# Optimization experiments

Hardware: AMD Instinct MI355X
Metric: run time of the kernel (lower is better)

The kernel has to match this reference:

```python
import jax, jax.numpy as jnp
import numpy as np

H, HKV, D = 16, 4, 64
ROPE_BASE = 10000.0
EPS = 1e-6


def _rms_norm(x):
    return x * jax.lax.rsqrt(jnp.mean(x * x, axis=-1, keepdims=True) + EPS)


def _rope_cos_sin(T, dtype):
    inv_freq = 1.0 / (ROPE_BASE ** (jnp.arange(0, D, 2, dtype=jnp.float32) / D))  # [D/2]
    t = jnp.arange(T, dtype=jnp.float32)
    freqs = jnp.outer(t, inv_freq)  # [T, D/2]
    return jnp.cos(freqs)[None, :, None, :].astype(dtype), jnp.sin(freqs)[None, :, None, :].astype(dtype)


def _apply_rope(x, cos, sin):
    d = x.shape[-1] // 2
    x1, x2 = x[..., :d], x[..., d:]
    return jnp.concatenate([x1 * cos + x2 * sin, -x1 * sin + x2 * cos], axis=-1)


def setup_inputs() -> dict:
    key = jax.random.key(0)
    ks = jax.random.split(key, 6)
    B, T, dm = 1, 2048, 1024
    x = jax.random.normal(ks[0], (B, T, dm), dtype=jnp.float32)
    q_w = jax.random.normal(ks[1], (H * D, dm), dtype=jnp.float32) * 0.02
    k_w = jax.random.normal(ks[2], (HKV * D, dm), dtype=jnp.float32) * 0.02
    v_w = jax.random.normal(ks[3], (HKV * D, dm), dtype=jnp.float32) * 0.02
    o_w = jax.random.normal(ks[4], (dm, H * D), dtype=jnp.float32) * 0.02
    temp = jnp.ones((H,), dtype=jnp.float32) * np.sqrt(D)  # per-head temperature buffer
    curvature = jnp.asarray(1.0, dtype=jnp.float32)
    return {"x": x, "q_w": q_w, "k_w": k_w, "v_w": v_w, "o_w": o_w, "temp": temp, "curvature": curvature}


def reference(x, q_w, k_w, v_w, o_w, temp, curvature):
    B, T, dm = x.shape
    # projections
    q = (x @ q_w.T).reshape(B, T, H, D)
    k = (x @ k_w.T).reshape(B, T, HKV, D)
    v = (x @ v_w.T).reshape(B, T, HKV, D)
    q, k = _rms_norm(q), _rms_norm(k)
    cos, sin = _rope_cos_sin(T, q.dtype)
    q = _apply_rope(q, cos, sin)
    k = _apply_rope(k, cos, sin)
    # GQA: repeat kv heads
    rep = H // HKV
    k = jnp.repeat(k, rep, axis=2)  # [B,T,H,D]
    v = jnp.repeat(v, rep, axis=2)
    c = curvature
    # hyperboloid lift: time component x0 = sqrt(1/c + ||x||^2)
    q0 = jnp.sqrt(1.0 / c + jnp.sum(q * q, axis=-1))  # [B,T,H]
    k0 = jnp.sqrt(1.0 / c + jnp.sum(k * k, axis=-1))
    # Minkowski inner product <q,k>_L = q.k_spatial - q0*k0  -> [B,H,Tq,Tk]
    mink = jnp.einsum('bqhd,bkhd->bhqk', q, k) - q0.transpose(0, 2, 1)[..., :, None] * k0.transpose(0, 2, 1)[..., None, :]
    # Lorentz distance d = arccosh(clamp(-c*<q,k>_L, 1+eps)) / sqrt(c)
    dist = jnp.arccosh(jnp.maximum(-c * mink, 1.0 + 1e-5)) / jnp.sqrt(c)
    scores = -dist / temp[None, :, None, None]
    causal = jnp.tril(jnp.ones((T, T), dtype=bool))
    scores = jnp.where(causal[None, None], scores, -jnp.inf)
    w = jax.nn.softmax(scores, axis=-1)  # [B,H,Tq,Tk]
    attn = jnp.einsum('bhqk,bkhd->bqhd', w, v).reshape(B, T, H * D)
    out = attn @ o_w.T  # [B,T,dm]
    spatial_norm = jnp.mean(jnp.sqrt(jnp.sum(q * q, axis=-1)))
    return out, spatial_norm
```

## Files before the change

kernel.cpp:

```cpp
#include <hip/hip_runtime.h>
#include <hip/hip_bf16.h>

typedef __attribute__((ext_vector_type(8))) short short8;
typedef __attribute__((ext_vector_type(4))) short bf16x4;
typedef __attribute__((ext_vector_type(4))) float f32x4;

#define TT 2048
#define DM 1024
#define NH 16
#define NKV 4
#define HD 64

#define MFMA32(a,b,c) __builtin_amdgcn_mfma_f32_16x16x32_bf16(a,b,c,0,0,0)
#define MFMA16(a,b,c) __builtin_amdgcn_mfma_f32_16x16x16bf16_1k(a,b,c,0,0,0)

__device__ __forceinline__ unsigned short f2bf(float x){
  unsigned int u = __float_as_uint(x);
  u += 0x7fffu + ((u >> 16) & 1u);
  return (unsigned short)(u >> 16);
}
__device__ __forceinline__ unsigned int pkbf2(float x, float y){
  union { __hip_bfloat162 h; unsigned int u; } t;
  t.h = __float22bfloat162_rn(make_float2(x, y));
  return t.u;
}

__global__ __launch_bounds__(256) void convertw_kernel(
    const float* __restrict__ x,
    const float* __restrict__ qw, const float* __restrict__ kw,
    const float* __restrict__ vw, const float* __restrict__ ow,
    unsigned short* __restrict__ xb,
    unsigned short* __restrict__ wqkv, unsigned short* __restrict__ owb){
  long v = (long)blockIdx.x * 256 + threadIdx.x;
  const float* src; unsigned short* dst; long base;
  if      (v < 524288) { src = x;  dst = xb;             base = v; }
  else if (v < 786432) { src = qw; dst = wqkv;           base = v - 524288; }
  else if (v < 851968) { src = kw; dst = wqkv + 1048576; base = v - 786432; }
  else if (v < 917504) { src = vw; dst = wqkv + 1310720; base = v - 851968; }
  else                 { src = ow; dst = owb;            base = v - 917504; }
  f32x4 d = *(const f32x4*)(src + base * 4);
  uint2 pk = { pkbf2(d[0], d[1]), pkbf2(d[2], d[3]) };
  *(uint2*)(dst + base * 4) = pk;
}

__global__ __launch_bounds__(256) void gemm1_fused(
    const unsigned short* __restrict__ xb, const unsigned short* __restrict__ wqkv,
    unsigned short* __restrict__ qb, unsigned short* __restrict__ kb,
    unsigned short* __restrict__ vt,
    float* __restrict__ q0, float* __restrict__ k0,
    float* __restrict__ bpart, const float* __restrict__ curv){
  __shared__ __align__(16) char smem_raw[18432];
  unsigned short* As = (unsigned short*)smem_raw;
  unsigned short* Bs = As + 64 * 72;
  float* Ct = (float*)smem_raw;
  __shared__ float bsum;
  const int tid = threadIdx.x, lane = tid & 63, wave = tid >> 6;
  const int hIdx = blockIdx.x;
  const int bm = blockIdx.y * 64, bn = hIdx * 64;
  const int wm = (wave >> 1) * 32, wn = (wave & 1) * 32;
  const int ml = lane & 15, quad = lane >> 4;
  if (tid == 0) bsum = 0.f;
  f32x4 acc[2][2];
  const f32x4 z = {0.f, 0.f, 0.f, 0.f};
  acc[0][0] = z; acc[0][1] = z; acc[1][0] = z; acc[1][1] = z;

  const int srow = tid >> 2, scol = (tid & 3) * 16;
  const unsigned short* Ag = xb + (long)(bm + srow) * 1024 + scol;
  const unsigned short* Bg = wqkv + (long)(bn + srow) * 1024 + scol;

  for (int kk = 0; kk < 1024; kk += 64){
    __syncthreads();
    *(uint4*)&As[srow * 72 + scol]     = *(const uint4*)(Ag + kk);
    *(uint4*)&As[srow * 72 + scol + 8] = *(const uint4*)(Ag + kk + 8);
    *(uint4*)&Bs[srow * 72 + scol]     = *(const uint4*)(Bg + kk);
    *(uint4*)&Bs[srow * 72 + scol + 8] = *(const uint4*)(Bg + kk + 8);
    __syncthreads();
#pragma unroll
    for (int ks = 0; ks < 64; ks += 32){
      short8 a0f = *(const short8*)&As[(wm + ml) * 72 + ks + quad * 8];
      short8 a1f = *(const short8*)&As[(wm + 16 + ml) * 72 + ks + quad * 8];
      short8 b0f = *(const short8*)&Bs[(wn + ml) * 72 + ks + quad * 8];
      short8 b1f = *(const short8*)&Bs[(wn + 16 + ml) * 72 + ks + quad * 8];
      acc[0][0] = MFMA32(a0f, b0f, acc[0][0]);
      acc[0][1] = MFMA32(a0f, b1f, acc[0][1]);
      acc[1][0] = MFMA32(a1f, b0f, acc[1][0]);
      acc[1][1] = MFMA32(a1f, b1f, acc[1][1]);
    }
  }
  __syncthreads();
#pragma unroll
  for (int i = 0; i < 2; i++)
#pragma unroll
    for (int j = 0; j < 2; j++)
#pragma unroll
      for (int r = 0; r < 4; r++)
        Ct[(wm + i * 16 + quad * 4 + r) * 65 + wn + j * 16 + ml] = acc[i][j][r];
  __syncthreads();

  if (hIdx < 20){
    const bool isq = hIdx < 16;
    const int h = isq ? hIdx : hIdx - 16;
    const float c = curv[0];
    unsigned short* ob = isq ? qb : kb;
    float* o0 = isq ? q0 : k0;
#pragma unroll 1
    for (int rr = 0; rr < 16; rr++){
      const int row = wave * 16 + rr;
      const int t = bm + row;
      float val = Ct[row * 65 + lane];
      float ss = val * val;
#pragma unroll
      for (int off = 1; off < 64; off <<= 1) ss += __shfl_xor(ss, off);
      float scale = __builtin_amdgcn_rsqf(ss * (1.f / 64.f) + 1e-6f);
      float xn = val * scale;
      float other = __shfl_xor(xn, 32);
      int fi = lane & 31;
      float ang = (float)t * __builtin_amdgcn_exp2f((float)fi * (-13.287712379549449f / 32.f));
      float sn, cs; __sincosf(ang, &sn, &cs);
      float outv = (lane < 32) ? (xn * cs + other * sn) : (xn * cs - other * sn);
      ob[((long)h * TT + t) * 64 + lane] = f2bf(outv);
      if (lane == 0){
        float sq = ss * scale * scale;
        o0[h * TT + t] = __builtin_amdgcn_sqrtf(1.f / c + sq);
        if (isq) atomicAdd(&bsum, __builtin_amdgcn_sqrtf(sq));
      }
    }
  } else {
    const int hk = hIdx - 20;
    const int d = tid >> 2, tseg = (tid & 3) * 16;
    uint4 w0, w1;
    w0.x = pkbf2(Ct[(tseg + 0) * 65 + d], Ct[(tseg + 1) * 65 + d]);
    w0.y = pkbf2(Ct[(tseg + 2) * 65 + d], Ct[(tseg + 3) * 65 + d]);
    w0.z = pkbf2(Ct[(tseg + 4) * 65 + d], Ct[(tseg + 5) * 65 + d]);
    w0.w = pkbf2(Ct[(tseg + 6) * 65 + d], Ct[(tseg + 7) * 65 + d]);
    w1.x = pkbf2(Ct[(tseg + 8) * 65 + d], Ct[(tseg + 9) * 65 + d]);
    w1.y = pkbf2(Ct[(tseg +10) * 65 + d], Ct[(tseg +11) * 65 + d]);
    w1.z = pkbf2(Ct[(tseg +12) * 65 + d], Ct[(tseg +13) * 65 + d]);
    w1.w = pkbf2(Ct[(tseg +14) * 65 + d], Ct[(tseg +15) * 65 + d]);
    const int tile = (bm + tseg) >> 4;
    unsigned short* dst = vt + ((long)(hk * 128 + tile) * 64 + d) * 16;
    *(uint4*)dst = w0;
    *(uint4*)(dst + 8) = w1;
  }
  __syncthreads();
  if (tid == 0) bpart[blockIdx.y * 24 + hIdx] = bsum;
}

__global__ __launch_bounds__(256, 3) void attn_kernel(
    const unsigned short* __restrict__ qb_, const unsigned short* __restrict__ kb_,
    const unsigned short* __restrict__ vt_,
    const float* __restrict__ q0_, const float* __restrict__ k0_,
    const float* __restrict__ temp, const float* __restrict__ curv,
    unsigned short* __restrict__ attn_out,
    const float* __restrict__ bpart, float* __restrict__ out_scalar){
  __shared__ float lds[8 * 1104];
  const int tid = threadIdx.x, lane = tid & 63, wave = tid >> 6;
  const int h = blockIdx.x & 15, pair = blockIdx.x >> 4;
  const int kvh = h >> 2;
  const int ml = lane & 15, quad = lane >> 4;
  const float c = curv[0];
  const float factor = -1.f / (__builtin_amdgcn_sqrtf(c) * temp[h]);
  const f32x4 z = {0.f, 0.f, 0.f, 0.f};
  const unsigned short* kh = kb_ + (long)kvh * TT * 64;
  const unsigned short* vh = vt_ + (long)kvh * 128 * 1024;
  const float* k0h = k0_ + kvh * TT;

  const int qtA = 127 - pair, qtB = pair;
  const int i0A = qtA * 16,   i0B = qtB * 16;
  short8 qa0 = *(const short8*)&qb_[((long)h * TT + i0A + ml) * 64 + quad * 8];
  short8 qa1 = *(const short8*)&qb_[((long)h * TT + i0A + ml) * 64 + 32 + quad * 8];
  short8 qb0 = *(const short8*)&qb_[((long)h * TT + i0B + ml) * 64 + quad * 8];
  short8 qb1 = *(const short8*)&qb_[((long)h * TT + i0B + ml) * 64 + 32 + quad * 8];
  const float q0cA = c * q0_[h * TT + i0A + ml];
  const float q0cB = c * q0_[h * TT + i0B + ml];
  const int rowqA = i0A + ml, rowqB = i0B + ml;

  f32x4 oA[4], oB[4];
#pragma unroll
  for (int dt = 0; dt < 4; dt++){ oA[dt] = z; oB[dt] = z; }
  float lA = 0.f, lB = 0.f;

  const int ntA = (i0A + 47) >> 5;
  const int ntB = (i0B + 47) >> 5;

#pragma unroll 1
  for (int t = wave; t < ntA; t += 4){
    const int j0 = t << 5;
    const unsigned short* kp = kh + (long)j0 * 64;
    short8 ka0 = *(const short8*)(kp + ml * 64 + quad * 8);
    short8 ka1 = *(const short8*)(kp + ml * 64 + 32 + quad * 8);
    short8 kc0 = *(const short8*)(kp + (16 + ml) * 64 + quad * 8);
    short8 kc1 = *(const short8*)(kp + (16 + ml) * 64 + 32 + quad * 8);
    f32x4 k0a = *(const f32x4*)(k0h + j0 + quad * 4);
    f32x4 k0b = *(const f32x4*)(k0h + j0 + 16 + quad * 4);
    const unsigned short* vpa = vh + (long)(j0 >> 4) * 1024;
    bf16x4 vfa0 = *(const bf16x4*)(vpa + ( 0 + ml) * 16 + quad * 4);
    bf16x4 vfa1 = *(const bf16x4*)(vpa + (16 + ml) * 16 + quad * 4);
    bf16x4 vfa2 = *(const bf16x4*)(vpa + (32 + ml) * 16 + quad * 4);
    bf16x4 vfa3 = *(const bf16x4*)(vpa + (48 + ml) * 16 + quad * 4);
    bf16x4 vfb0 = *(const bf16x4*)(vpa + 1024 + ( 0 + ml) * 16 + quad * 4);
    bf16x4 vfb1 = *(const bf16x4*)(vpa + 1024 + (16 + ml) * 16 + quad * 4);
    bf16x4 vfb2 = *(const bf16x4*)(vpa + 1024 + (32 + ml) * 16 + quad * 4);
    bf16x4 vfb3 = *(const bf16x4*)(vpa + 1024 + (48 + ml) * 16 + quad * 4);

    const int keyb = j0 + quad * 4;
    {
      f32x4 s0 = z, s1 = z;
      s0 = MFMA32(ka0, qa0, s0);
      s0 = MFMA32(ka1, qa1, s0);
      s1 = MFMA32(kc0, qa0, s1);
      s1 = MFMA32(kc1, qa1, s1);
      const bool nm = (j0 + 31 > i0A);
      float p0[4], p1[4];
#pragma unroll
      for (int r = 0; r < 4; r++){
        float argA = fmaxf(__builtin_fmaf(-c, s0[r], q0cA * k0a[r]), 1.00001f);
        float wA   = argA + __builtin_amdgcn_sqrtf(__builtin_fmaf(argA, argA, -1.f));
        float pA   = __builtin_amdgcn_exp2f(factor * __builtin_amdgcn_logf(wA));
        float argB = fmaxf(__builtin_fmaf(-c, s1[r], q0cA * k0b[r]), 1.00001f);
        float wB   = argB + __builtin_amdgcn_sqrtf(__builtin_fmaf(argB, argB, -1.f));
        float pB   = __builtin_amdgcn_exp2f(factor * __builtin_amdgcn_logf(wB));
        if (nm){
          if (keyb + r > rowqA)      pA = 0.f;
          if (keyb + 16 + r > rowqA) pB = 0.f;
        }
        p0[r] = pA; p1[r] = pB;
        lA += pA + pB;
      }
      uint2 pua = { pkbf2(p0[0], p0[1]), pkbf2(p0[2], p0[3]) };
      uint2 pub = { pkbf2(p1[0], p1[1]), pkbf2(p1[2], p1[3]) };
      bf16x4 pfa = *(bf16x4*)&pua;
      bf16x4 pfb = *(bf16x4*)&pub;
      oA[0] = MFMA16(vfa0, pfa, oA[0]);
      oA[1] = MFMA16(vfa1, pfa, oA[1]);
      oA[2] = MFMA16(vfa2, pfa, oA[2]);
      oA[3] = MFMA16(vfa3, pfa, oA[3]);
      oA[0] = MFMA16(vfb0, pfb, oA[0]);
      oA[1] = MFMA16(vfb1, pfb, oA[1]);
      oA[2] = MFMA16(vfb2, pfb, oA[2]);
      oA[3] = MFMA16(vfb3, pfb, oA[3]);
    }
    if (t < ntB){
      f32x4 s0 = z, s1 = z;
      s0 = MFMA32(ka0, qb0, s0);
      s0 = MFMA32(ka1, qb1, s0);
      s1 = MFMA32(kc0, qb0, s1);
      s1 = MFMA32(kc1, qb1, s1);
      const bool nm = (j0 + 31 > i0B);
      float p0[4], p1[4];
#pragma unroll
      for (int r = 0; r < 4; r++){
        float argA = fmaxf(__builtin_fmaf(-c, s0[r], q0cB * k0a[r]), 1.00001f);
        float wA   = argA + __builtin_amdgcn_sqrtf(__builtin_fmaf(argA, argA, -1.f));
        float pA   = __builtin_amdgcn_exp2f(factor * __builtin_amdgcn_logf(wA));
        float argB = fmaxf(__builtin_fmaf(-c, s1[r], q0cB * k0b[r]), 1.00001f);
        float wB   = argB + __builtin_amdgcn_sqrtf(__builtin_fmaf(argB, argB, -1.f));
        float pB   = __builtin_amdgcn_exp2f(factor * __builtin_amdgcn_logf(wB));
        if (nm){
          if (keyb + r > rowqB)      pA = 0.f;
          if (keyb + 16 + r > rowqB) pB = 0.f;
        }
        p0[r] = pA; p1[r] = pB;
        lB += pA + pB;
      }
      uint2 pua = { pkbf2(p0[0], p0[1]), pkbf2(p0[2], p0[3]) };
      uint2 pub = { pkbf2(p1[0], p1[1]), pkbf2(p1[2], p1[3]) };
      bf16x4 pfa = *(bf16x4*)&pua;
      bf16x4 pfb = *(bf16x4*)&pub;
      oB[0] = MFMA16(vfa0, pfa, oB[0]);
      oB[1] = MFMA16(vfa1, pfa, oB[1]);
      oB[2] = MFMA16(vfa2, pfa, oB[2]);
      oB[3] = MFMA16(vfa3, pfa, oB[3]);
      oB[0] = MFMA16(vfb0, pfb, oB[0]);
      oB[1] = MFMA16(vfb1, pfb, oB[1]);
      oB[2] = MFMA16(vfb2, pfb, oB[2]);
      oB[3] = MFMA16(vfb3, pfb, oB[3]);
    }
  }
  lA += __shfl_xor(lA, 16); lA += __shfl_xor(lA, 32);
  lB += __shfl_xor(lB, 16); lB += __shfl_xor(lB, 32);
  {
    float* wA = lds + wave * 1104;
    float* wB = lds + (4 + wave) * 1104;
#pragma unroll
    for (int dt = 0; dt < 4; dt++){
      *(f32x4*)&wA[ml * 68 + dt * 16 + quad * 4] = oA[dt];
      *(f32x4*)&wB[ml * 68 + dt * 16 + quad * 4] = oB[dt];
    }
    if (quad == 0){ wA[1088 + ml] = lA; wB[1088 + ml] = lB; }
  }
  __syncthreads();
  {
    const int row = tid >> 4, c0 = (tid & 15) * 4;
#pragma unroll 1
    for (int tb = 0; tb < 2; tb++){
      const float* base = lds + tb * 4 * 1104;
      float L = 0.f; f32x4 s = z;
#pragma unroll
      for (int w = 0; w < 4; w++){
        const float* rg = base + w * 1104;
        L += rg[1088 + row];
        f32x4 t2 = *(const f32x4*)&rg[row * 68 + c0];
        s[0] += t2[0]; s[1] += t2[1]; s[2] += t2[2]; s[3] += t2[3];
      }
      float invL = __builtin_amdgcn_rcpf(L);
      const int i0 = tb ? i0B : i0A;
      uint2 o = { pkbf2(s[0] * invL, s[1] * invL), pkbf2(s[2] * invL, s[3] * invL) };
      *(uint2*)&attn_out[(long)(i0 + row) * 1024 + h * 64 + c0] = o;
    }
  }
  if (blockIdx.x == 0 && tid < 64){
    float s = 0.f;
    for (int i = lane; i < 768; i += 64) s += bpart[i];
#pragma unroll
    for (int off = 1; off < 64; off <<= 1) s += __shfl_xor(s, off);
    if (lane == 0) out_scalar[0] = s * (1.f / 32768.f);
  }
}

__global__ __launch_bounds__(256) void gemm2_kernel(
    const unsigned short* __restrict__ A, const unsigned short* __restrict__ B,
    float* __restrict__ C){
  __shared__ __align__(16) unsigned short As[64 * 72];
  __shared__ __align__(16) unsigned short Bs[64 * 72];
  const int tid = threadIdx.x, lane = tid & 63, wave = tid >> 6;
  const int bm = blockIdx.y * 64, bn = blockIdx.x * 64;
  const int wm = (wave >> 1) * 32, wn = (wave & 1) * 32;
  const int ml = lane & 15, quad = lane >> 4;
  f32x4 acc[2][2];
  const f32x4 z = {0.f, 0.f, 0.f, 0.f};
  acc[0][0] = z; acc[0][1] = z; acc[1][0] = z; acc[1][1] = z;

  const int srow = tid >> 2, scol = (tid & 3) * 16;
  const unsigned short* Ag = A + (long)(bm + srow) * 1024 + scol;
  const unsigned short* Bg = B + (long)(bn + srow) * 1024 + scol;

  for (int kk = 0; kk < 1024; kk += 64){
    __syncthreads();
    *(uint4*)&As[srow * 72 + scol]     = *(const uint4*)(Ag + kk);
    *(uint4*)&As[srow * 72 + scol + 8] = *(const uint4*)(Ag + kk + 8);
    *(uint4*)&Bs[srow * 72 + scol]     = *(const uint4*)(Bg + kk);
    *(uint4*)&Bs[srow * 72 + scol + 8] = *(const uint4*)(Bg + kk + 8);
    __syncthreads();
#pragma unroll
    for (int ks = 0; ks < 64; ks += 32){
      short8 a0f = *(const short8*)&As[(wm + ml) * 72 + ks + quad * 8];
      short8 a1f = *(const short8*)&As[(wm + 16 + ml) * 72 + ks + quad * 8];
      short8 b0f = *(const short8*)&Bs[(wn + ml) * 72 + ks + quad * 8];
      short8 b1f = *(const short8*)&Bs[(wn + 16 + ml) * 72 + ks + quad * 8];
      acc[0][0] = MFMA32(a0f, b0f, acc[0][0]);
      acc[0][1] = MFMA32(a0f, b1f, acc[0][1]);
      acc[1][0] = MFMA32(a1f, b0f, acc[1][0]);
      acc[1][1] = MFMA32(a1f, b1f, acc[1][1]);
    }
  }
#pragma unroll
  for (int i = 0; i < 2; i++)
#pragma unroll
    for (int j = 0; j < 2; j++)
#pragma unroll
      for (int r = 0; r < 4; r++)
        C[(long)(bm + wm + i * 16 + quad * 4 + r) * 1024 + bn + wn + j * 16 + ml] = acc[i][j][r];
}

extern "C" void kernel_launch(void* const* d_in, const int* in_sizes, int n_in,
                              void* d_out, int out_size, void* d_ws, size_t ws_size,
                              hipStream_t stream){
  const float* x    = (const float*)d_in[0];
  const float* qw   = (const float*)d_in[1];
  const float* kw   = (const float*)d_in[2];
  const float* vw   = (const float*)d_in[3];
  const float* ow   = (const float*)d_in[4];
  const float* temp = (const float*)d_in[5];
  const float* curv = (const float*)d_in[6];
  float* out = (float*)d_out;

  char* ws = (char*)d_ws;
  size_t off = 0;
  auto alloc = [&](size_t bytes) -> char* {
    char* p = ws + off;
    off += (bytes + 255) & ~(size_t)255;
    return p;
  };
  unsigned short* xb   = (unsigned short*)alloc((size_t)TT * DM * 2);
  unsigned short* wqkv = (unsigned short*)alloc((size_t)1536 * DM * 2);
  unsigned short* owb  = (unsigned short*)alloc((size_t)DM * DM * 2);
  unsigned short* qb   = (unsigned short*)alloc((size_t)NH * TT * HD * 2);
  unsigned short* kb   = (unsigned short*)alloc((size_t)NKV * TT * HD * 2);
  unsigned short* vt   = (unsigned short*)alloc((size_t)NKV * TT * HD * 2);
  float*          q0   = (float*)alloc((size_t)NH * TT * 4);
  float*          k0   = (float*)alloc((size_t)NKV * TT * 4);
  unsigned short* attn = (unsigned short*)alloc((size_t)TT * DM * 2);
  float*          bpart= (float*)alloc((size_t)768 * 4);

  convertw_kernel<<<4608, 256, 0, stream>>>(x, qw, kw, vw, ow, xb, wqkv, owb);
  gemm1_fused<<<dim3(24, 32), 256, 0, stream>>>(xb, wqkv, qb, kb, vt, q0, k0, bpart, curv);
  attn_kernel<<<1024, 256, 0, stream>>>(qb, kb, vt, q0, k0, temp, curv, attn,
                                        bpart, out + (size_t)TT * DM);
  gemm2_kernel<<<dim3(16, 32), 256, 0, stream>>>(attn, owb, out);
}
```

Before: 174.4 us.

## Pair two GQA query heads per block instead of two causal query tiles

Result: faster. 159.5 us (-8.5%).

```diff
diff --git a/kernel.cpp b/kernel.cpp
--- a/kernel.cpp
+++ b/kernel.cpp
@@ -155,36 +155,38 @@
     const float* __restrict__ bpart, float* __restrict__ out_scalar){
   __shared__ float lds[8 * 1104];
   const int tid = threadIdx.x, lane = tid & 63, wave = tid >> 6;
-  const int h = blockIdx.x & 15, pair = blockIdx.x >> 4;
-  const int kvh = h >> 2;
+  const int qt  = 127 - (blockIdx.x >> 3);
+  const int sub = blockIdx.x & 7;
+  const int kvh = sub >> 1, hp = sub & 1;
+  const int h0 = kvh * 4 + hp * 2, h1 = h0 + 1;
+  const int i0 = qt * 16;
   const int ml = lane & 15, quad = lane >> 4;
   const float c = curv[0];
-  const float factor = -1.f / (__builtin_amdgcn_sqrtf(c) * temp[h]);
+  const float rsc = __builtin_amdgcn_rsqf(c);
+  const float fac0 = -rsc / temp[h0];
+  const float fac1 = -rsc / temp[h1];
   const f32x4 z = {0.f, 0.f, 0.f, 0.f};
   const unsigned short* kh = kb_ + (long)kvh * TT * 64;
   const unsigned short* vh = vt_ + (long)kvh * 128 * 1024;
   const float* k0h = k0_ + kvh * TT;
 
-  const int qtA = 127 - pair, qtB = pair;
-  const int i0A = qtA * 16,   i0B = qtB * 16;
-  short8 qa0 = *(const short8*)&qb_[((long)h * TT + i0A + ml) * 64 + quad * 8];
-  short8 qa1 = *(const short8*)&qb_[((long)h * TT + i0A + ml) * 64 + 32 + quad * 8];
-  short8 qb0 = *(const short8*)&qb_[((long)h * TT + i0B + ml) * 64 + quad * 8];
-  short8 qb1 = *(const short8*)&qb_[((long)h * TT + i0B + ml) * 64 + 32 + quad * 8];
-  const float q0cA = c * q0_[h * TT + i0A + ml];
-  const float q0cB = c * q0_[h * TT + i0B + ml];
-  const int rowqA = i0A + ml, rowqB = i0B + ml;
-
-  f32x4 oA[4], oB[4];
-#pragma unroll
-  for (int dt = 0; dt < 4; dt++){ oA[dt] = z; oB[dt] = z; }
-  float lA = 0.f, lB = 0.f;
-
-  const int ntA = (i0A + 47) >> 5;
-  const int ntB = (i0B + 47) >> 5;
+  short8 qa0 = *(const short8*)&qb_[((long)h0 * TT + i0 + ml) * 64 + quad * 8];
+  short8 qa1 = *(const short8*)&qb_[((long)h0 * TT + i0 + ml) * 64 + 32 + quad * 8];
+  short8 qb0 = *(const short8*)&qb_[((long)h1 * TT + i0 + ml) * 64 + quad * 8];
+  short8 qb1 = *(const short8*)&qb_[((long)h1 * TT + i0 + ml) * 64 + 32 + quad * 8];
+  const float q0c0 = c * q0_[h0 * TT + i0 + ml];
+  const float q0c1 = c * q0_[h1 * TT + i0 + ml];
+  const int rowq = i0 + ml;
+
+  f32x4 o0[4], o1[4];
+#pragma unroll
+  for (int dt = 0; dt < 4; dt++){ o0[dt] = z; o1[dt] = z; }
+  float l0 = 0.f, l1 = 0.f;
+
+  const int nt = (i0 + 47) >> 5;
 
 #pragma unroll 1
-  for (int t = wave; t < ntA; t += 4){
+  for (int t = wave; t < nt; t += 4){
     const int j0 = t << 5;
     const unsigned short* kp = kh + (long)j0 * 64;
     short8 ka0 = *(const short8*)(kp + ml * 64 + quad * 8);
@@ -204,97 +206,96 @@
     bf16x4 vfb3 = *(const bf16x4*)(vpa + 1024 + (48 + ml) * 16 + quad * 4);
 
     const int keyb = j0 + quad * 4;
+    const bool nm = (j0 + 31 > i0);
     {
       f32x4 s0 = z, s1 = z;
       s0 = MFMA32(ka0, qa0, s0);
       s0 = MFMA32(ka1, qa1, s0);
       s1 = MFMA32(kc0, qa0, s1);
       s1 = MFMA32(kc1, qa1, s1);
-      const bool nm = (j0 + 31 > i0A);
       float p0[4], p1[4];
 #pragma unroll
       for (int r = 0; r < 4; r++){
-        float argA = fmaxf(__builtin_fmaf(-c, s0[r], q0cA * k0a[r]), 1.00001f);
+        float argA = fmaxf(__builtin_fmaf(-c, s0[r], q0c0 * k0a[r]), 1.00001f);
         float wA   = argA + __builtin_amdgcn_sqrtf(__builtin_fmaf(argA, argA, -1.f));
-        float pA   = __builtin_amdgcn_exp2f(factor * __builtin_amdgcn_logf(wA));
-        float argB = fmaxf(__builtin_fmaf(-c, s1[r], q0cA * k0b[r]), 1.00001f);
+        float pA   = __builtin_amdgcn_exp2f(fac0 * __builtin_amdgcn_logf(wA));
+        float argB = fmaxf(__builtin_fmaf(-c, s1[r], q0c0 * k0b[r]), 1.00001f);
         float wB   = argB + __builtin_amdgcn_sqrtf(__builtin_fmaf(argB, argB, -1.f));
-        float pB   = __builtin_amdgcn_exp2f(factor * __builtin_amdgcn_logf(wB));
+        float pB   = __builtin_amdgcn_exp2f(fac0 * __builtin_amdgcn_logf(wB));
         if (nm){
-          if (keyb + r > rowqA)      pA = 0.f;
-          if (keyb + 16 + r > rowqA) pB = 0.f;
+          if (keyb + r > rowq)      pA = 0.f;
+          if (keyb + 16 + r > rowq) pB = 0.f;
         }
         p0[r] = pA; p1[r] = pB;
-        lA += pA + pB;
+        l0 += pA + pB;
       }
       uint2 pua = { pkbf2(p0[0], p0[1]), pkbf2(p0[2], p0[3]) };
       uint2 pub = { pkbf2(p1[0], p1[1]), pkbf2(p1[2], p1[3]) };
       bf16x4 pfa = *(bf16x4*)&pua;
       bf16x4 pfb = *(bf16x4*)&pub;
-      oA[0] = MFMA16(vfa0, pfa, oA[0]);
-      oA[1] = MFMA16(vfa1, pfa, oA[1]);
-      oA[2] = MFMA16(vfa2, pfa, oA[2]);
-      oA[3] = MFMA16(vfa3, pfa, oA[3]);
-      oA[0] = MFMA16(vfb0, pfb, oA[0]);
-      oA[1] = MFMA16(vfb1, pfb, oA[1]);
-      oA[2] = MFMA16(vfb2, pfb, oA[2]);
-      oA[3] = MFMA16(vfb3, pfb, oA[3]);
-    }
-    if (t < ntB){
+      o0[0] = MFMA16(vfa0, pfa, o0[0]);
+      o0[1] = MFMA16(vfa1, pfa, o0[1]);
+      o0[2] = MFMA16(vfa2, pfa, o0[2]);
+      o0[3] = MFMA16(vfa3, pfa, o0[3]);
+      o0[0] = MFMA16(vfb0, pfb, o0[0]);
+      o0[1] = MFMA16(vfb1, pfb, o0[1]);
+      o0[2] = MFMA16(vfb2, pfb, o0[2]);
+      o0[3] = MFMA16(vfb3, pfb, o0[3]);
+    }
+    {
       f32x4 s0 = z, s1 = z;
       s0 = MFMA32(ka0, qb0, s0);
       s0 = MFMA32(ka1, qb1, s0);
       s1 = MFMA32(kc0, qb0, s1);
       s1 = MFMA32(kc1, qb1, s1);
-      const bool nm = (j0 + 31 > i0B);
       float p0[4], p1[4];
 #pragma unroll
       for (int r = 0; r < 4; r++){
-        float argA = fmaxf(__builtin_fmaf(-c, s0[r], q0cB * k0a[r]), 1.00001f);
+        float argA = fmaxf(__builtin_fmaf(-c, s0[r], q0c1 * k0a[r]), 1.00001f);
         float wA   = argA + __builtin_amdgcn_sqrtf(__builtin_fmaf(argA, argA, -1.f));
-        float pA   = __builtin_amdgcn_exp2f(factor * __builtin_amdgcn_logf(wA));
-        float argB = fmaxf(__builtin_fmaf(-c, s1[r], q0cB * k0b[r]), 1.00001f);
+        float pA   = __builtin_amdgcn_exp2f(fac1 * __builtin_amdgcn_logf(wA));
+        float argB = fmaxf(__builtin_fmaf(-c, s1[r], q0c1 * k0b[r]), 1.00001f);
         float wB   = argB + __builtin_amdgcn_sqrtf(__builtin_fmaf(argB, argB, -1.f));
-        float pB   = __builtin_amdgcn_exp2f(factor * __builtin_amdgcn_logf(wB));
+        float pB   = __builtin_amdgcn_exp2f(fac1 * __builtin_amdgcn_logf(wB));
         if (nm){
-          if (keyb + r > rowqB)      pA = 0.f;
-          if (keyb + 16 + r > rowqB) pB = 0.f;
+          if (keyb + r > rowq)      pA = 0.f;
+          if (keyb + 16 + r > rowq) pB = 0.f;
         }
         p0[r] = pA; p1[r] = pB;
-        lB += pA + pB;
+        l1 += pA + pB;
       }
       uint2 pua = { pkbf2(p0[0], p0[1]), pkbf2(p0[2], p0[3]) };
       uint2 pub = { pkbf2(p1[0], p1[1]), pkbf2(p1[2], p1[3]) };
       bf16x4 pfa = *(bf16x4*)&pua;
       bf16x4 pfb = *(bf16x4*)&pub;
-      oB[0] = MFMA16(vfa0, pfa, oB[0]);
-      oB[1] = MFMA16(vfa1, pfa, oB[1]);
-      oB[2] = MFMA16(vfa2, pfa, oB[2]);
-      oB[3] = MFMA16(vfa3, pfa, oB[3]);
-      oB[0] = MFMA16(vfb0, pfb, oB[0]);
-      oB[1] = MFMA16(vfb1, pfb, oB[1]);
-      oB[2] = MFMA16(vfb2, pfb, oB[2]);
-      oB[3] = MFMA16(vfb3, pfb, oB[3]);
-    }
-  }
-  lA += __shfl_xor(lA, 16); lA += __shfl_xor(lA, 32);
-  lB += __shfl_xor(lB, 16); lB += __shfl_xor(lB, 32);
+      o1[0] = MFMA16(vfa0, pfa, o1[0]);
+      o1[1] = MFMA16(vfa1, pfa, o1[1]);
+      o1[2] = MFMA16(vfa2, pfa, o1[2]);
+      o1[3] = MFMA16(vfa3, pfa, o1[3]);
+      o1[0] = MFMA16(vfb0, pfb, o1[0]);
+      o1[1] = MFMA16(vfb1, pfb, o1[1]);
+      o1[2] = MFMA16(vfb2, pfb, o1[2]);
+      o1[3] = MFMA16(vfb3, pfb, o1[3]);
+    }
+  }
+  l0 += __shfl_xor(l0, 16); l0 += __shfl_xor(l0, 32);
+  l1 += __shfl_xor(l1, 16); l1 += __shfl_xor(l1, 32);
   {
-    float* wA = lds + wave * 1104;
-    float* wB = lds + (4 + wave) * 1104;
+    float* w0 = lds + wave * 1104;
+    float* w1 = lds + (4 + wave) * 1104;
 #pragma unroll
     for (int dt = 0; dt < 4; dt++){
-      *(f32x4*)&wA[ml * 68 + dt * 16 + quad * 4] = oA[dt];
-      *(f32x4*)&wB[ml * 68 + dt * 16 + quad * 4] = oB[dt];
-    }
-    if (quad == 0){ wA[1088 + ml] = lA; wB[1088 + ml] = lB; }
+      *(f32x4*)&w0[ml * 68 + dt * 16 + quad * 4] = o0[dt];
+      *(f32x4*)&w1[ml * 68 + dt * 16 + quad * 4] = o1[dt];
+    }
+    if (quad == 0){ w0[1088 + ml] = l0; w1[1088 + ml] = l1; }
   }
   __syncthreads();
   {
     const int row = tid >> 4, c0 = (tid & 15) * 4;
 #pragma unroll 1
-    for (int tb = 0; tb < 2; tb++){
-      const float* base = lds + tb * 4 * 1104;
+    for (int hb = 0; hb < 2; hb++){
+      const float* base = lds + hb * 4 * 1104;
       float L = 0.f; f32x4 s = z;
 #pragma unroll
       for (int w = 0; w < 4; w++){
@@ -304,7 +305,7 @@
         s[0] += t2[0]; s[1] += t2[1]; s[2] += t2[2]; s[3] += t2[3];
       }
       float invL = __builtin_amdgcn_rcpf(L);
-      const int i0 = tb ? i0B : i0A;
+      const int h = hb ? h1 : h0;
       uint2 o = { pkbf2(s[0] * invL, s[1] * invL), pkbf2(s[2] * invL, s[3] * invL) };
       *(uint2*)&attn_out[(long)(i0 + row) * 1024 + h * 64 + c0] = o;
     }
```
